# Performance work log

Hardware: AMD Instinct MI355X
Metric: run time of the kernel (lower is better)

Reference implementation:

```python
import jax, jax.numpy as jnp
import numpy as np

EPS = 1e-5

def _bn(x, p):
    # eval-mode BatchNorm over the last (channel) axis; p = [gamma, beta, mean, var]
    g, b, m, v = p[0], p[1], p[2], p[3]
    return (x - m) * jax.lax.rsqrt(v + EPS) * g + b

def _mk_bn(key, c):
    kg, kb, km, kv = jax.random.split(key, 4)
    return jnp.stack([
        jax.random.uniform(kg, (c,), minval=0.5, maxval=1.5),
        jax.random.normal(kb, (c,)) * 0.1,
        jax.random.normal(km, (c,)) * 0.1,
        jax.random.uniform(kv, (c,), minval=0.5, maxval=1.5),
    ]).astype(jnp.float32)

def setup_inputs() -> dict:
    key = jax.random.key(0)
    ks = jax.random.split(key, 12)
    B, N, K = 2, 65536, 16
    IN_CH, OUT_CH = 32, 128
    D = IN_CH + 3            # 35
    C16 = OUT_CH // 16       # 8
    C4 = OUT_CH // 4         # 32
    G = 1                    # num_group
    feats = jax.random.normal(ks[0], (B, N, D), dtype=jnp.float32)
    idx = jax.random.randint(ks[1], (B, N, K), 0, N, dtype=jnp.int64)
    s = lambda fi, fo: (2.0 / fi) ** 0.5
    return {
        "features": feats,
        "idx": idx,
        "point_W": jax.random.normal(ks[2], (10, C16), dtype=jnp.float32) * s(10, C16),
        "point_bn": _mk_bn(ks[3], C16),
        "eta_W": jax.random.normal(ks[4], (IN_CH, C16), dtype=jnp.float32) * s(IN_CH, C16),
        "eta_bn": _mk_bn(ks[5], C16),
        "mu_W": jax.random.normal(ks[6], (IN_CH, C16), dtype=jnp.float32) * s(IN_CH, C16),
        "mu_bn": _mk_bn(ks[7], C16),
        "gamma_W": jax.random.normal(ks[8], (D, C4), dtype=jnp.float32) * s(D, C4),
        "gamma_bn": _mk_bn(ks[9], C4),
        "map_W": jax.random.normal(ks[10], (3 * C16, G), dtype=jnp.float32) * s(3 * C16, G),
        "map_bn": _mk_bn(ks[10], G),
        "fc_W": jax.random.normal(ks[11], (C4, OUT_CH), dtype=jnp.float32) * s(C4, OUT_CH),
    }

def reference(features, idx, point_W, point_bn, eta_W, eta_bn, mu_W, mu_bn,
              gamma_W, gamma_bn, map_W, map_bn, fc_W):
    # features: [B,N,D] (D = 3 xyz + in_channel), idx: [B,N,K] kNN indices
    nbr = jax.vmap(lambda f, i: f[i])(features, idx)     # [B,N,K,D] gather
    pn = nbr[..., :3]                                    # neighbor xyz
    pnf = nbr[..., 3:]                                   # neighbor feats
    feat = features[..., 3:]                             # center feats [B,N,Cin]
    p = features[:, :, None, :3]                         # center xyz, bcast over K
    diff = p - pn
    point = jnp.concatenate([
        jnp.sum(diff * diff, axis=-1, keepdims=True),
        jnp.broadcast_to(p, pn.shape), pn, diff,
    ], axis=-1)                                          # [B,N,K,10]
    point = jax.nn.relu(_bn(point @ point_W, point_bn))  # [B,N,K,C16]
    eta = _bn((feat @ eta_W)[:, :, None, :], eta_bn)     # [B,N,1,C16] (repeat over K)
    mu = _bn(pnf @ mu_W, mu_bn)                          # [B,N,K,C16]
    feature = jnp.concatenate([jnp.broadcast_to(eta, mu.shape), mu], axis=-1)  # concat mode
    feature = jnp.concatenate([point, feature], axis=-1)                       # [B,N,K,3*C16]
    feature = jax.nn.relu(_bn(feature @ map_W, map_bn))  # [B,N,K,G]
    gam = _bn(nbr @ gamma_W, gamma_bn)                   # [B,N,K,C4]
    rep = gam.shape[-1] // feature.shape[-1]             # out/4 / num_group
    feature = jnp.tile(feature, (1, 1, 1, rep))          # channel repeat
    out = jnp.max(feature * gam, axis=2)                 # max over neighbors -> [B,N,C4]
    return out @ fc_W                                    # [B,N,out_channel]
```

## Files before the change

### kernel.cpp

```cpp
#include <hip/hip_runtime.h>
#include <hip/hip_fp16.h>
#include <math.h>

#define N_PTS   65536
#define BATCH   2
#define TOTAL   (BATCH * N_PTS)
#define NPACK_DW 16
#define CPACK   12
#define EPSB    1e-5f

typedef float  f32x4  __attribute__((ext_vector_type(4)));
typedef _Float16 f16x8 __attribute__((ext_vector_type(8)));

static __device__ inline unsigned h2u(float a, float b) {
    __half2 h = __floats2half2_rn(a, b);
    union { __half2 h; unsigned u; } cv; cv.h = h; return cv.u;
}
static __device__ inline float2 u2f2(unsigned u) {
    union { unsigned u; __half2 h; } cv; cv.u = u; return __half22float2(cv.h);
}
static __device__ inline unsigned pk_max(unsigned a, unsigned b) {
    unsigned r; asm("v_pk_max_f16 %0, %1, %2" : "=v"(r) : "v"(a), "v"(b)); return r;
}
static __device__ inline unsigned pk_fma(unsigned a, unsigned b, unsigned c) {
    unsigned r; asm("v_pk_fma_f16 %0, %1, %2, %3" : "=v"(r) : "v"(a), "v"(b), "v"(c)); return r;
}
static __device__ inline unsigned pkrtz(float a, float b) {
    unsigned r; asm("v_cvt_pkrtz_f16_f32 %0, %1, %2" : "=v"(r) : "v"(a), "v"(b)); return r;
}

__global__ __launch_bounds__(256) void k1_precompute(
    const float* __restrict__ feats,
    const float* __restrict__ pW,
    const float* __restrict__ pBN,
    const float* __restrict__ eW,
    const float* __restrict__ eBN,
    const float* __restrict__ mW,
    const float* __restrict__ mBN,
    const float* __restrict__ gW,
    const float* __restrict__ gBN,
    const float* __restrict__ mapW,
    const float* __restrict__ mapBN,
    const float* __restrict__ fcW,
    unsigned* __restrict__ packN,
    float* __restrict__ packC,
    unsigned* __restrict__ fc16,
    float* __restrict__ gateC)
{
    __shared__ float sG[35 * 32];
    __shared__ float sE[32 * 8];
    __shared__ float sM[32 * 8];

    const int tid = threadIdx.x;
    const int j = blockIdx.x * 256 + tid;

    float f[36];
    {
        const float* row = feats + (size_t)j * 35;
#pragma unroll
        for (int q4 = 0; q4 < 8; ++q4) {
            const float4 v = *(const float4*)(row + q4 * 4);
            f[q4 * 4 + 0] = v.x; f[q4 * 4 + 1] = v.y;
            f[q4 * 4 + 2] = v.z; f[q4 * 4 + 3] = v.w;
        }
        const float4 v = *(const float4*)(row + 31);
        f[31] = v.x; f[32] = v.y; f[33] = v.z; f[34] = v.w;
    }

    for (int i = tid; i < 1120; i += 256) sG[i] = gW[i];
    sE[tid] = eW[tid];
    sM[tid] = mW[tid];
    __syncthreads();

    const float x = f[0], y = f[1], z = f[2];
    const float pp = x * x + y * y + z * z;

    float G[32];
#pragma unroll
    for (int q = 0; q < 32; ++q) G[q] = 0.f;
#pragma unroll 5
    for (int d = 0; d < 35; ++d) {
        const float fd = f[d];
        const float4* w4 = (const float4*)(sG + d * 32);
#pragma unroll
        for (int q4 = 0; q4 < 8; ++q4) {
            const float4 w = w4[q4];
            G[q4 * 4 + 0] = fmaf(fd, w.x, G[q4 * 4 + 0]);
            G[q4 * 4 + 1] = fmaf(fd, w.y, G[q4 * 4 + 1]);
            G[q4 * 4 + 2] = fmaf(fd, w.z, G[q4 * 4 + 2]);
            G[q4 * 4 + 3] = fmaf(fd, w.w, G[q4 * 4 + 3]);
        }
    }
#pragma unroll
    for (int q = 0; q < 32; ++q) {
        const float g = gBN[q], b = gBN[32 + q], m = gBN[64 + q], v = gBN[96 + q];
        const float s = g / sqrtf(v + EPSB);
        G[q] = fmaf(G[q], s, b - m * s);
    }

    float eta[8], mu[8];
#pragma unroll
    for (int q = 0; q < 8; ++q) { eta[q] = 0.f; mu[q] = 0.f; }
#pragma unroll 4
    for (int i = 0; i < 32; ++i) {
        const float fi = f[3 + i];
        const float4* e4 = (const float4*)(sE + i * 8);
        const float4* m4 = (const float4*)(sM + i * 8);
#pragma unroll
        for (int h = 0; h < 2; ++h) {
            const float4 we = e4[h], wm = m4[h];
            eta[h * 4 + 0] = fmaf(fi, we.x, eta[h * 4 + 0]);
            eta[h * 4 + 1] = fmaf(fi, we.y, eta[h * 4 + 1]);
            eta[h * 4 + 2] = fmaf(fi, we.z, eta[h * 4 + 2]);
            eta[h * 4 + 3] = fmaf(fi, we.w, eta[h * 4 + 3]);
            mu[h * 4 + 0] = fmaf(fi, wm.x, mu[h * 4 + 0]);
            mu[h * 4 + 1] = fmaf(fi, wm.y, mu[h * 4 + 1]);
            mu[h * 4 + 2] = fmaf(fi, wm.z, mu[h * 4 + 2]);
            mu[h * 4 + 3] = fmaf(fi, wm.w, mu[h * 4 + 3]);
        }
    }
    float etadot = 0.f, Mdot = 0.f;
#pragma unroll
    for (int q = 0; q < 8; ++q) {
        const float ge = eBN[q], be = eBN[8 + q], me = eBN[16 + q], ve = eBN[24 + q];
        const float se = ge / sqrtf(ve + EPSB);
        etadot = fmaf(fmaf(eta[q], se, be - me * se), mapW[8 + q], etadot);
        const float gm = mBN[q], bm = mBN[8 + q], mm = mBN[16 + q], vm = mBN[24 + q];
        const float sm = gm / sqrtf(vm + EPSB);
        Mdot = fmaf(fmaf(mu[q], sm, bm - mm * sm), mapW[16 + q], Mdot);
    }

    float Bnp[8], Ap[8];
#pragma unroll
    for (int q = 0; q < 8; ++q) {
        const float pw0 = pW[q];
        const float g = pBN[q], b = pBN[8 + q], m = pBN[16 + q], v = pBN[24 + q];
        const float s = g / sqrtf(v + EPSB);
        const float t = b - m * s;
        const float Braw = pp * pw0
            + x * (pW[32 + q] - pW[56 + q])
            + y * (pW[40 + q] - pW[64 + q])
            + z * (pW[48 + q] - pW[72 + q]);
        const float Araw = pp * pw0
            + x * (pW[8 + q]  + pW[56 + q])
            + y * (pW[16 + q] + pW[64 + q])
            + z * (pW[24 + q] + pW[72 + q]);
        Bnp[q] = Braw * s;
        Ap[q]  = fmaf(Araw, s, t);
    }

    float gmax = 0.f;
#pragma unroll
    for (int q = 0; q < 32; ++q) gmax = fmaxf(gmax, fabsf(G[q]));
    const float inv = (gmax > 0.f) ? (127.f / gmax) : 0.f;
    unsigned gq[8];
#pragma unroll
    for (int qd = 0; qd < 8; ++qd) {
        const unsigned u0 = (unsigned)((int)rintf(G[4*qd+0] * inv) + 128) & 0xffu;
        const unsigned u1 = (unsigned)((int)rintf(G[4*qd+1] * inv) + 128) & 0xffu;
        const unsigned u2 = (unsigned)((int)rintf(G[4*qd+2] * inv) + 128) & 0xffu;
        const unsigned u3 = (unsigned)((int)rintf(G[4*qd+3] * inv) + 128) & 0xffu;
        gq[qd] = u0 | (u2 << 8) | (u1 << 16) | (u3 << 24);
    }
    union { float f; unsigned u; } sc; sc.f = gmax;

    uint4* PN = (uint4*)(packN + (size_t)j * NPACK_DW);
    PN[0] = make_uint4(h2u(x, y), h2u(z, Mdot), h2u(Bnp[0], Bnp[1]), h2u(Bnp[2], Bnp[3]));
    PN[1] = make_uint4(h2u(Bnp[4], Bnp[5]), h2u(Bnp[6], Bnp[7]), gq[0], gq[1]);
    PN[2] = make_uint4(gq[2], gq[3], gq[4], gq[5]);
    PN[3] = make_uint4(gq[6], gq[7], sc.u, 0u);

    float4* PC = (float4*)(packC + (size_t)j * CPACK);
    PC[0] = make_float4(x, y, z, etadot);
    PC[1] = make_float4(Ap[0], Ap[1], Ap[2], Ap[3]);
    PC[2] = make_float4(Ap[4], Ap[5], Ap[6], Ap[7]);

    if (blockIdx.x == 0) {
        for (int fi = tid; fi < 512; fi += 256) {
            const int lm = fi & 15, nt = (fi >> 4) & 7, lq = fi >> 7;
            unsigned dws[4];
#pragma unroll
            for (int p = 0; p < 4; ++p) {
                const float a = fcW[(8 * lq + 2 * p)     * 128 + nt * 16 + lm];
                const float b = fcW[(8 * lq + 2 * p + 1) * 128 + nt * 16 + lm];
                dws[p] = h2u(a, b);
            }
            ((uint4*)fc16)[fi] = make_uint4(dws[0], dws[1], dws[2], dws[3]);
        }
        if (tid == 0) {
#pragma unroll
            for (int q = 0; q < 8; ++q) {
                const float g = pBN[q], v = pBN[24 + q];
                const float s = g / sqrtf(v + EPSB);
                gateC[q]     = 2.f * pW[q] * s;
                gateC[8 + q] = mapW[q];
            }
            const float g = mapBN[0], b = mapBN[1], m = mapBN[2], v = mapBN[3];
            const float ms = g / sqrtf(v + EPSB);
            gateC[16] = ms;
            gateC[17] = b - m * ms;
        }
    }
}

__global__ __launch_bounds__(256) void k2_aggregate_fc(
    const int* __restrict__ idx,
    const unsigned* __restrict__ packN,
    const float* __restrict__ packC,
    const unsigned* __restrict__ fc16,
    const float* __restrict__ gateC,
    float* __restrict__ out)
{
    __shared__ __align__(16) unsigned short sPool[32 * 40];

    const int bid  = blockIdx.x;
    const int xcd  = bid & 7, slot = bid >> 3;
    const int cb   = (xcd < 4) ? (slot * 4 + xcd)
                               : (2048 + slot * 4 + (xcd - 4));
    const int cbase = cb * 32;

    const int tid  = threadIdx.x;
    const int cl   = tid >> 3;
    const int ks   = tid & 7;
    const int c    = cbase + cl;
    const int lane = tid & 63;
    const int w    = tid >> 6;
    const int lm   = lane & 15, lq = lane >> 4;

    f16x8 bfrag[2];
#pragma unroll
    for (int ntj = 0; ntj < 2; ++ntj) {
        union { uint4 u4; f16x8 v; } cv;
        cv.u4 = ((const uint4*)fc16)[(lq * 8 + 2 * w + ntj) * 16 + lm];
        bfrag[ntj] = cv.v;
    }

    const float ms = gateC[16], mt = gateC[17];
    float W0p[8], mW0[8];
#pragma unroll
    for (int q = 0; q < 8; ++q) { W0p[q] = gateC[q]; mW0[q] = gateC[8 + q]; }

    const float4* PC = (const float4*)(packC + (size_t)c * CPACK);
    const float4 c0 = PC[0], c1 = PC[1], c2 = PC[2];
    const float px = c0.x, py = c0.y, pz = c0.z, etadot = c0.w;
    const float Ap[8] = { c1.x, c1.y, c1.z, c1.w, c2.x, c2.y, c2.z, c2.w };

    const int2 ib2 = ((const int2*)idx)[c * 8 + ks];
    const int bbase = c & ~(N_PTS - 1);

    unsigned o16[16];
#pragma unroll
    for (int q = 0; q < 16; ++q) o16[q] = 0xFC00FC00u;

    const uint4* P0 = (const uint4*)(packN + (size_t)(bbase + ib2.x) * NPACK_DW);
    const uint4* P1 = (const uint4*)(packN + (size_t)(bbase + ib2.y) * NPACK_DW);
    uint4 n0[4] = { P0[0], P0[1], P0[2], P0[3] };
    uint4 n1[4] = { P1[0], P1[1], P1[2], P1[3] };

#pragma unroll
    for (int k = 0; k < 2; ++k) {
        const uint4* N = k ? n1 : n0;
        const float2 xy = u2f2(N[0].x), zM = u2f2(N[0].y);
        const float dot3 = px * xy.x + py * xy.y + pz * zM.x;

        const unsigned bn[4] = { N[0].z, N[0].w, N[1].x, N[1].y };
        float pd = 0.f;
#pragma unroll
        for (int q = 0; q < 4; ++q) {
            const float2 bn2 = u2f2(bn[q]);
            const float u0 = Ap[2 * q]     + bn2.x - dot3 * W0p[2 * q];
            const float u1 = Ap[2 * q + 1] + bn2.y - dot3 * W0p[2 * q + 1];
            pd = fmaf(fmaxf(u0, 0.f), mW0[2 * q], pd);
            pd = fmaf(fmaxf(u1, 0.f), mW0[2 * q + 1], pd);
        }
        float s = fmaf(pd + etadot + zM.y, ms, mt);
        s = fmaxf(s, 0.f);

        union { unsigned u; float f; } sc; sc.u = N[3].z;
        const float t = s * sc.f * (1.f / 127.f);
        const unsigned t2 = pkrtz(t, t);
        const float d = -1152.f * t;
        const unsigned d2 = pkrtz(d, d);

        const unsigned gd[8] = { N[1].z, N[1].w, N[2].x, N[2].y,
                                 N[2].z, N[2].w, N[3].x, N[3].y };
#pragma unroll
        for (int qd = 0; qd < 8; ++qd) {
            const unsigned dwv = gd[qd];
            const unsigned lo = (dwv & 0x00FF00FFu) | 0x64006400u;
            const unsigned hi = ((dwv >> 8) & 0x00FF00FFu) | 0x64006400u;
            o16[2 * qd]     = pk_max(o16[2 * qd],     pk_fma(lo, t2, d2));
            o16[2 * qd + 1] = pk_max(o16[2 * qd + 1], pk_fma(hi, t2, d2));
        }
    }

#pragma unroll
    for (int q = 0; q < 16; ++q) {
        unsigned v = o16[q];
        v = pk_max(v, (unsigned)__shfl_xor((int)v, 1));
        v = pk_max(v, (unsigned)__shfl_xor((int)v, 2));
        v = pk_max(v, (unsigned)__shfl_xor((int)v, 4));
        o16[q] = v;
    }

    {
        uint2 pk;
        pk.x = o16[2 * ks];
        pk.y = o16[2 * ks + 1];
        *(uint2*)(sPool + cl * 40 + ks * 4) = pk;
    }
    __syncthreads();

    f32x4 acc[2][2];
#pragma unroll
    for (int a = 0; a < 2; ++a)
#pragma unroll
        for (int b = 0; b < 2; ++b)
            acc[a][b] = (f32x4){0.f, 0.f, 0.f, 0.f};

#pragma unroll
    for (int mtile = 0; mtile < 2; ++mtile) {
        const f16x8 afrag = *(const f16x8*)(sPool + (mtile * 16 + lm) * 40 + lq * 8);
#pragma unroll
        for (int ntj = 0; ntj < 2; ++ntj)
            acc[mtile][ntj] = __builtin_amdgcn_mfma_f32_16x16x32_f16(
                afrag, bfrag[ntj], acc[mtile][ntj], 0, 0, 0);
    }

#pragma unroll
    for (int mtile = 0; mtile < 2; ++mtile)
#pragma unroll
        for (int ntj = 0; ntj < 2; ++ntj) {
            const int nt = 2 * w + ntj;
#pragma unroll
            for (int r = 0; r < 4; ++r)
                __builtin_nontemporal_store(acc[mtile][ntj][r],
                    &out[(size_t)(cbase + mtile * 16 + lq * 4 + r) * 128 + nt * 16 + lm]);
        }
}

extern "C" void kernel_launch(void* const* d_in, const int* in_sizes, int n_in,
                              void* d_out, int out_size, void* d_ws, size_t ws_size,
                              hipStream_t stream) {
    const float* feats    = (const float*)d_in[0];
    const int*   idx      = (const int*)  d_in[1];
    const float* point_W  = (const float*)d_in[2];
    const float* point_bn = (const float*)d_in[3];
    const float* eta_W    = (const float*)d_in[4];
    const float* eta_bn   = (const float*)d_in[5];
    const float* mu_W     = (const float*)d_in[6];
    const float* mu_bn    = (const float*)d_in[7];
    const float* gamma_W  = (const float*)d_in[8];
    const float* gamma_bn = (const float*)d_in[9];
    const float* map_W    = (const float*)d_in[10];
    const float* map_bn   = (const float*)d_in[11];
    const float* fc_W     = (const float*)d_in[12];
    float* out = (float*)d_out;

    unsigned* packN = (unsigned*)d_ws;
    float*    packC = (float*)(packN + (size_t)TOTAL * NPACK_DW);
    unsigned* fc16  = (unsigned*)(packC + (size_t)TOTAL * CPACK);
    float*    gateC = (float*)(fc16 + 2048);

    hipLaunchKernelGGL(k1_precompute, dim3(TOTAL / 256), dim3(256), 0, stream,
                       feats, point_W, point_bn, eta_W, eta_bn, mu_W, mu_bn,
                       gamma_W, gamma_bn, map_W, map_bn, fc_W,
                       packN, packC, fc16, gateC);
    hipLaunchKernelGGL(k2_aggregate_fc, dim3(TOTAL / 32), dim3(256), 0, stream,
                       idx, packN, packC, fc16, gateC, out);
}
```

Measured before the change: 168.2 us.

## Compute per-point projections in k1 with MFMA 16x16x32 f16 tiles

The precompute kernel stops giving each thread one point with scalar FMA loops over LDS-staged weights. Each wavefront now handles 16 points and runs the gamma, eta and mu projections as f16 MFMA instructions, with the xyz terms added in fp32. The packed outputs are staged in LDS and written back with coalesced uint4 stores, and the grid grows to four times as many blocks. This cuts the VALU work and uncoalesced stores in k1, but the projection inputs and weights are now rounded to f16, which lowers precision.

```diff
diff --git a/kernel.cpp b/kernel.cpp
--- a/kernel.cpp
+++ b/kernel.cpp
@@ -47,153 +47,156 @@
     unsigned* __restrict__ fc16,
     float* __restrict__ gateC)
 {
-    __shared__ float sG[35 * 32];
-    __shared__ float sE[32 * 8];
-    __shared__ float sM[32 * 8];
-
-    const int tid = threadIdx.x;
-    const int j = blockIdx.x * 256 + tid;
-
-    float f[36];
+    __shared__ __align__(16) unsigned char sPk[4][1792];
+
+    const int tid  = threadIdx.x;
+    const int lane = tid & 63, wv = tid >> 6;
+    const int lm   = lane & 15, lq = lane >> 4;
+    const int pt0  = blockIdx.x * 64 + wv * 16;
+
+    f16x8 bG0, bG1, bEM;
     {
-        const float* row = feats + (size_t)j * 35;
-#pragma unroll
-        for (int q4 = 0; q4 < 8; ++q4) {
-            const float4 v = *(const float4*)(row + q4 * 4);
-            f[q4 * 4 + 0] = v.x; f[q4 * 4 + 1] = v.y;
-            f[q4 * 4 + 2] = v.z; f[q4 * 4 + 3] = v.w;
-        }
-        const float4 v = *(const float4*)(row + 31);
-        f[31] = v.x; f[32] = v.y; f[33] = v.z; f[34] = v.w;
-    }
-
-    for (int i = tid; i < 1120; i += 256) sG[i] = gW[i];
-    sE[tid] = eW[tid];
-    sM[tid] = mW[tid];
-    __syncthreads();
-
-    const float x = f[0], y = f[1], z = f[2];
-    const float pp = x * x + y * y + z * z;
-
-    float G[32];
-#pragma unroll
-    for (int q = 0; q < 32; ++q) G[q] = 0.f;
-#pragma unroll 5
-    for (int d = 0; d < 35; ++d) {
-        const float fd = f[d];
-        const float4* w4 = (const float4*)(sG + d * 32);
-#pragma unroll
-        for (int q4 = 0; q4 < 8; ++q4) {
-            const float4 w = w4[q4];
-            G[q4 * 4 + 0] = fmaf(fd, w.x, G[q4 * 4 + 0]);
-            G[q4 * 4 + 1] = fmaf(fd, w.y, G[q4 * 4 + 1]);
-            G[q4 * 4 + 2] = fmaf(fd, w.z, G[q4 * 4 + 2]);
-            G[q4 * 4 + 3] = fmaf(fd, w.w, G[q4 * 4 + 3]);
-        }
-    }
-#pragma unroll
-    for (int q = 0; q < 32; ++q) {
-        const float g = gBN[q], b = gBN[32 + q], m = gBN[64 + q], v = gBN[96 + q];
-        const float s = g / sqrtf(v + EPSB);
-        G[q] = fmaf(G[q], s, b - m * s);
-    }
-
-    float eta[8], mu[8];
-#pragma unroll
-    for (int q = 0; q < 8; ++q) { eta[q] = 0.f; mu[q] = 0.f; }
-#pragma unroll 4
-    for (int i = 0; i < 32; ++i) {
-        const float fi = f[3 + i];
-        const float4* e4 = (const float4*)(sE + i * 8);
-        const float4* m4 = (const float4*)(sM + i * 8);
-#pragma unroll
-        for (int h = 0; h < 2; ++h) {
-            const float4 we = e4[h], wm = m4[h];
-            eta[h * 4 + 0] = fmaf(fi, we.x, eta[h * 4 + 0]);
-            eta[h * 4 + 1] = fmaf(fi, we.y, eta[h * 4 + 1]);
-            eta[h * 4 + 2] = fmaf(fi, we.z, eta[h * 4 + 2]);
-            eta[h * 4 + 3] = fmaf(fi, we.w, eta[h * 4 + 3]);
-            mu[h * 4 + 0] = fmaf(fi, wm.x, mu[h * 4 + 0]);
-            mu[h * 4 + 1] = fmaf(fi, wm.y, mu[h * 4 + 1]);
-            mu[h * 4 + 2] = fmaf(fi, wm.z, mu[h * 4 + 2]);
-            mu[h * 4 + 3] = fmaf(fi, wm.w, mu[h * 4 + 3]);
-        }
-    }
-    float etadot = 0.f, Mdot = 0.f;
-#pragma unroll
-    for (int q = 0; q < 8; ++q) {
-        const float ge = eBN[q], be = eBN[8 + q], me = eBN[16 + q], ve = eBN[24 + q];
-        const float se = ge / sqrtf(ve + EPSB);
-        etadot = fmaf(fmaf(eta[q], se, be - me * se), mapW[8 + q], etadot);
-        const float gm = mBN[q], bm = mBN[8 + q], mm = mBN[16 + q], vm = mBN[24 + q];
-        const float sm = gm / sqrtf(vm + EPSB);
-        Mdot = fmaf(fmaf(mu[q], sm, bm - mm * sm), mapW[16 + q], Mdot);
-    }
-
-    float Bnp[8], Ap[8];
-#pragma unroll
-    for (int q = 0; q < 8; ++q) {
-        const float pw0 = pW[q];
-        const float g = pBN[q], b = pBN[8 + q], m = pBN[16 + q], v = pBN[24 + q];
-        const float s = g / sqrtf(v + EPSB);
-        const float t = b - m * s;
-        const float Braw = pp * pw0
-            + x * (pW[32 + q] - pW[56 + q])
-            + y * (pW[40 + q] - pW[64 + q])
-            + z * (pW[48 + q] - pW[72 + q]);
-        const float Araw = pp * pw0
-            + x * (pW[8 + q]  + pW[56 + q])
-            + y * (pW[16 + q] + pW[64 + q])
-            + z * (pW[24 + q] + pW[72 + q]);
-        Bnp[q] = Braw * s;
-        Ap[q]  = fmaf(Araw, s, t);
-    }
-
-    float gmax = 0.f;
-#pragma unroll
-    for (int q = 0; q < 32; ++q) gmax = fmaxf(gmax, fabsf(G[q]));
-    const float inv = (gmax > 0.f) ? (127.f / gmax) : 0.f;
-    unsigned gq[8];
-#pragma unroll
-    for (int qd = 0; qd < 8; ++qd) {
-        const unsigned u0 = (unsigned)((int)rintf(G[4*qd+0] * inv) + 128) & 0xffu;
-        const unsigned u1 = (unsigned)((int)rintf(G[4*qd+1] * inv) + 128) & 0xffu;
-        const unsigned u2 = (unsigned)((int)rintf(G[4*qd+2] * inv) + 128) & 0xffu;
-        const unsigned u3 = (unsigned)((int)rintf(G[4*qd+3] * inv) + 128) & 0xffu;
-        gq[qd] = u0 | (u2 << 8) | (u1 << 16) | (u3 << 24);
-    }
-    union { float f; unsigned u; } sc; sc.f = gmax;
-
-    uint4* PN = (uint4*)(packN + (size_t)j * NPACK_DW);
-    PN[0] = make_uint4(h2u(x, y), h2u(z, Mdot), h2u(Bnp[0], Bnp[1]), h2u(Bnp[2], Bnp[3]));
-    PN[1] = make_uint4(h2u(Bnp[4], Bnp[5]), h2u(Bnp[6], Bnp[7]), gq[0], gq[1]);
-    PN[2] = make_uint4(gq[2], gq[3], gq[4], gq[5]);
-    PN[3] = make_uint4(gq[6], gq[7], sc.u, 0u);
-
-    float4* PC = (float4*)(packC + (size_t)j * CPACK);
-    PC[0] = make_float4(x, y, z, etadot);
-    PC[1] = make_float4(Ap[0], Ap[1], Ap[2], Ap[3]);
-    PC[2] = make_float4(Ap[4], Ap[5], Ap[6], Ap[7]);
+        union { unsigned short u[8]; f16x8 v; } c0, c1, c2;
+#pragma unroll
+        for (int j = 0; j < 8; ++j) {
+            const int k = 8 * lq + j;
+            c0.u[j] = __half_as_ushort(__float2half_rn(gW[(3 + k) * 32 + lm]));
+            c1.u[j] = __half_as_ushort(__float2half_rn(gW[(3 + k) * 32 + 16 + lm]));
+            const float w2 = (lm < 8) ? eW[k * 8 + lm] : mW[k * 8 + (lm - 8)];
+            c2.u[j] = __half_as_ushort(__float2half_rn(w2));
+        }
+        bG0 = c0.v; bG1 = c1.v; bEM = c2.v;
+    }
+    const float sA = gBN[lm]      / sqrtf(gBN[96 + lm]  + EPSB);
+    const float tA = gBN[32 + lm] - gBN[64 + lm] * sA;
+    const float sB = gBN[16 + lm] / sqrtf(gBN[112 + lm] + EPSB);
+    const float tB = gBN[48 + lm] - gBN[80 + lm] * sB;
+    const float w0a = gW[lm],      w1a = gW[32 + lm],      w2a = gW[64 + lm];
+    const float w0b = gW[16 + lm], w1b = gW[48 + lm],      w2b = gW[80 + lm];
+    float sE_, tE_, mpw;
+    if (lm < 8) {
+        sE_ = eBN[lm] / sqrtf(eBN[24 + lm] + EPSB);
+        tE_ = eBN[8 + lm] - eBN[16 + lm] * sE_;
+        mpw = mapW[8 + lm];
+    } else {
+        const int qq = lm - 8;
+        sE_ = mBN[qq] / sqrtf(mBN[24 + qq] + EPSB);
+        tE_ = mBN[8 + qq] - mBN[16 + qq] * sE_;
+        mpw = mapW[16 + qq];
+    }
+    const int  q   = lm & 7;
+    const bool isB = lm < 8;
+    const float pw0 = pW[q];
+    const float sp  = pBN[q] / sqrtf(pBN[24 + q] + EPSB);
+    const float tp  = pBN[8 + q] - pBN[16 + q] * sp;
+    float cxx, cyy, czz;
+    if (isB) { cxx = pW[32+q]-pW[56+q]; cyy = pW[40+q]-pW[64+q]; czz = pW[48+q]-pW[72+q]; }
+    else     { cxx = pW[8+q] +pW[56+q]; cyy = pW[16+q]+pW[64+q]; czz = pW[24+q]+pW[72+q]; }
+
+    f16x8 afrag;
+    {
+        const float* ar = feats + (size_t)(pt0 + lm) * 35 + 3 + 8 * lq;
+        const float4 a0 = *(const float4*)ar;
+        const float4 a1 = *(const float4*)(ar + 4);
+        union { unsigned u[4]; f16x8 v; } cv;
+        cv.u[0] = h2u(a0.x, a0.y); cv.u[1] = h2u(a0.z, a0.w);
+        cv.u[2] = h2u(a1.x, a1.y); cv.u[3] = h2u(a1.z, a1.w);
+        afrag = cv.v;
+    }
+    float X[4], Y[4], Z[4], PP[4];
+#pragma unroll
+    for (int r = 0; r < 4; ++r) {
+        const float* rr = feats + (size_t)(pt0 + 4 * lq + r) * 35;
+        X[r] = rr[0]; Y[r] = rr[1]; Z[r] = rr[2];
+        PP[r] = X[r]*X[r] + Y[r]*Y[r] + Z[r]*Z[r];
+    }
+
+    f32x4 aG0 = {0.f,0.f,0.f,0.f}, aG1 = {0.f,0.f,0.f,0.f}, aEM = {0.f,0.f,0.f,0.f};
+    aG0 = __builtin_amdgcn_mfma_f32_16x16x32_f16(afrag, bG0, aG0, 0, 0, 0);
+    aG1 = __builtin_amdgcn_mfma_f32_16x16x32_f16(afrag, bG1, aG1, 0, 0, 0);
+    aEM = __builtin_amdgcn_mfma_f32_16x16x32_f16(afrag, bEM, aEM, 0, 0, 0);
+
+    float G0[4], G1[4], eD[4], mD[4], BA[4], gm[4], iv[4];
+#pragma unroll
+    for (int r = 0; r < 4; ++r) {
+        G0[r] = fmaf(aG0[r] + X[r]*w0a + Y[r]*w1a + Z[r]*w2a, sA, tA);
+        G1[r] = fmaf(aG1[r] + X[r]*w0b + Y[r]*w1b + Z[r]*w2b, sB, tB);
+        float v = fmaf(aEM[r], sE_, tE_) * mpw;
+        v += __shfl_xor(v, 1);
+        v += __shfl_xor(v, 2);
+        v += __shfl_xor(v, 4);
+        const float o = __shfl_xor(v, 8);
+        eD[r] = isB ? v : o;
+        mD[r] = isB ? o : v;
+        const float raw = PP[r]*pw0 + X[r]*cxx + Y[r]*cyy + Z[r]*czz;
+        BA[r] = isB ? raw * sp : fmaf(raw, sp, tp);
+        float m = fmaxf(fabsf(G0[r]), fabsf(G1[r]));
+        m = fmaxf(m, __shfl_xor(m, 1));
+        m = fmaxf(m, __shfl_xor(m, 2));
+        m = fmaxf(m, __shfl_xor(m, 4));
+        m = fmaxf(m, __shfl_xor(m, 8));
+        gm[r] = m;
+        iv[r] = (m > 0.f) ? (127.f / m) : 0.f;
+    }
+
+    unsigned char* PNl = sPk[wv];
+    unsigned char* PCl = sPk[wv] + 1024;
+    const int pos = (0x3120 >> ((lm & 3) * 4)) & 0xF;
+    const int gb0 = 24 + ((lm >> 2) << 2) + pos;
+#pragma unroll
+    for (int r = 0; r < 4; ++r) {
+        const int row = 4 * lq + r;
+        unsigned char* RN = PNl + row * 64;
+        RN[gb0]      = (unsigned char)((int)rintf(G0[r] * iv[r]) + 128);
+        RN[gb0 + 16] = (unsigned char)((int)rintf(G1[r] * iv[r]) + 128);
+        if (isB) {
+            *(unsigned short*)(RN + 8 + 2 * q) =
+                __half_as_ushort(__float2half_rn(BA[r]));
+        } else {
+            *(float*)(PCl + row * 48 + 16 + 4 * q) = BA[r];
+        }
+        if (lm == 0)
+            *(float4*)(PCl + row * 48) = make_float4(X[r], Y[r], Z[r], eD[r]);
+        if (lm == 1) {
+            *(unsigned*)(RN + 0) = h2u(X[r], Y[r]);
+            *(unsigned*)(RN + 4) = h2u(Z[r], mD[r]);
+        }
+        if (lm == 2) {
+            union { float f; unsigned u; } sc; sc.f = gm[r];
+            *(unsigned*)(RN + 56) = sc.u;
+            *(unsigned*)(RN + 60) = 0u;
+        }
+    }
+
+    {
+        const uint4 v = *(const uint4*)(PNl + (lane >> 2) * 64 + (lane & 3) * 16);
+        ((uint4*)packN)[(size_t)(pt0 + (lane >> 2)) * 4 + (lane & 3)] = v;
+    }
+    if (lane < 48) {
+        const int pr = lane / 3, pc = lane % 3;
+        const uint4 v = *(const uint4*)(PCl + pr * 48 + pc * 16);
+        ((uint4*)packC)[(size_t)(pt0 + pr) * 3 + pc] = v;
+    }
 
     if (blockIdx.x == 0) {
         for (int fi = tid; fi < 512; fi += 256) {
-            const int lm = fi & 15, nt = (fi >> 4) & 7, lq = fi >> 7;
+            const int flm = fi & 15, nt = (fi >> 4) & 7, flq = fi >> 7;
             unsigned dws[4];
 #pragma unroll
             for (int p = 0; p < 4; ++p) {
-                const float a = fcW[(8 * lq + 2 * p)     * 128 + nt * 16 + lm];
-                const float b = fcW[(8 * lq + 2 * p + 1) * 128 + nt * 16 + lm];
+                const float a = fcW[(8 * flq + 2 * p)     * 128 + nt * 16 + flm];
+                const float b = fcW[(8 * flq + 2 * p + 1) * 128 + nt * 16 + flm];
                 dws[p] = h2u(a, b);
             }
             ((uint4*)fc16)[fi] = make_uint4(dws[0], dws[1], dws[2], dws[3]);
         }
         if (tid == 0) {
 #pragma unroll
-            for (int q = 0; q < 8; ++q) {
-                const float g = pBN[q], v = pBN[24 + q];
+            for (int qq = 0; qq < 8; ++qq) {
+                const float g = pBN[qq], v = pBN[24 + qq];
                 const float s = g / sqrtf(v + EPSB);
-                gateC[q]     = 2.f * pW[q] * s;
-                gateC[8 + q] = mapW[q];
+                gateC[qq]     = 2.f * pW[qq] * s;
+                gateC[8 + qq] = mapW[qq];
             }
             const float g = mapBN[0], b = mapBN[1], m = mapBN[2], v = mapBN[3];
             const float ms = g / sqrtf(v + EPSB);
@@ -238,7 +241,7 @@
     const float ms = gateC[16], mt = gateC[17];
     float W0p[8], mW0[8];
 #pragma unroll
-    for (int q = 0; q < 8; ++q) { W0p[q] = gateC[q]; mW0[q] = gateC[8 + q]; }
+    for (int qq = 0; qq < 8; ++qq) { W0p[qq] = gateC[qq]; mW0[qq] = gateC[8 + qq]; }
 
     const float4* PC = (const float4*)(packC + (size_t)c * CPACK);
     const float4 c0 = PC[0], c1 = PC[1], c2 = PC[2];
@@ -250,7 +253,7 @@
 
     unsigned o16[16];
 #pragma unroll
-    for (int q = 0; q < 16; ++q) o16[q] = 0xFC00FC00u;
+    for (int qq = 0; qq < 16; ++qq) o16[qq] = 0xFC00FC00u;
 
     const uint4* P0 = (const uint4*)(packN + (size_t)(bbase + ib2.x) * NPACK_DW);
     const uint4* P1 = (const uint4*)(packN + (size_t)(bbase + ib2.y) * NPACK_DW);
@@ -266,12 +269,12 @@
         const unsigned bn[4] = { N[0].z, N[0].w, N[1].x, N[1].y };
         float pd = 0.f;
 #pragma unroll
-        for (int q = 0; q < 4; ++q) {
-            const float2 bn2 = u2f2(bn[q]);
-            const float u0 = Ap[2 * q]     + bn2.x - dot3 * W0p[2 * q];
-            const float u1 = Ap[2 * q + 1] + bn2.y - dot3 * W0p[2 * q + 1];
-            pd = fmaf(fmaxf(u0, 0.f), mW0[2 * q], pd);
-            pd = fmaf(fmaxf(u1, 0.f), mW0[2 * q + 1], pd);
+        for (int qq = 0; qq < 4; ++qq) {
+            const float2 bn2 = u2f2(bn[qq]);
+            const float u0 = Ap[2 * qq]     + bn2.x - dot3 * W0p[2 * qq];
+            const float u1 = Ap[2 * qq + 1] + bn2.y - dot3 * W0p[2 * qq + 1];
+            pd = fmaf(fmaxf(u0, 0.f), mW0[2 * qq], pd);
+            pd = fmaf(fmaxf(u1, 0.f), mW0[2 * qq + 1], pd);
         }
         float s = fmaf(pd + etadot + zM.y, ms, mt);
         s = fmaxf(s, 0.f);
@@ -295,12 +298,12 @@
     }
 
 #pragma unroll
-    for (int q = 0; q < 16; ++q) {
-        unsigned v = o16[q];
+    for (int qq = 0; qq < 16; ++qq) {
+        unsigned v = o16[qq];
         v = pk_max(v, (unsigned)__shfl_xor((int)v, 1));
         v = pk_max(v, (unsigned)__shfl_xor((int)v, 2));
         v = pk_max(v, (unsigned)__shfl_xor((int)v, 4));
-        o16[q] = v;
+        o16[qq] = v;
     }
 
     {
@@ -362,7 +365,7 @@
     unsigned* fc16  = (unsigned*)(packC + (size_t)TOTAL * CPACK);
     float*    gateC = (float*)(fc16 + 2048);
 
-    hipLaunchKernelGGL(k1_precompute, dim3(TOTAL / 256), dim3(256), 0, stream,
+    hipLaunchKernelGGL(k1_precompute, dim3(TOTAL / 64), dim3(256), 0, stream,
                        feats, point_W, point_bn, eta_W, eta_bn, mu_W, mu_bn,
                        gamma_W, gamma_bn, map_W, map_bn, fc_W,
                        packN, packC, fc16, gateC);
```

Result: faster. 146.2 us (-13.1%).
